# Optimization experiments

Hardware: AMD Instinct MI355X
Metric: run time of the kernel (lower is better)

Reference implementation:

```python
import jax, jax.numpy as jnp
import numpy as np

VOCAB_SIZE = 50000

def setup_inputs() -> dict:
    key = jax.random.key(0)
    # token index sequences: [batch, seq_len], values in [0, vocab)
    x = jax.random.randint(key, (2048, 200), 0, VOCAB_SIZE, dtype=jnp.int64)
    return {"x": x}

def reference(x) -> jnp.ndarray:
    # Faithful to: sum_{l} one_hot(x[b, l], V)  ->  [batch, vocab] count histogram.
    # Implemented as a scatter-add instead of materializing the
    # [batch, seq_len, vocab] one-hot tensor (same math, O(B*L) traffic on the
    # index side plus the [B, V] output).
    B, L = x.shape
    rows = jnp.broadcast_to(jnp.arange(B)[:, None], (B, L))  # [B, L]
    out = jnp.zeros((B, VOCAB_SIZE), dtype=jnp.float32)
    out = out.at[rows, x].add(jnp.float32(1.0))
    return out
```

## Files before the change

kernel.cpp:

```cpp
#include <hip/hip_runtime.h>
#include <hip/hip_bf16.h>

#define VOCAB   50000
#define SEQ     200
#define NCHUNK  4
#define CHUNK   (VOCAB / NCHUNK)
#define CDW     (CHUNK / 4)
#define CDW_PAD 3136

typedef float v4f __attribute__((ext_vector_type(4)));
typedef unsigned v4u __attribute__((ext_vector_type(4)));

__global__ __launch_bounds__(256) void MultihotEmbedding_16458314678493_kernel(
    const int* __restrict__ x, float* __restrict__ out) {
  __shared__ unsigned cnt[CDW_PAD];

  v4u* __restrict__ c4 = (v4u*)cnt;
  const v4u z = {0u, 0u, 0u, 0u};
  for (int i = threadIdx.x; i < CDW_PAD / 4; i += 256) c4[i] = z;
  __syncthreads();

  const int row = blockIdx.x >> 2;
  const int lo  = (blockIdx.x & 3) * CHUNK;
  const int* __restrict__ xr = x + row * SEQ;

  for (int t = threadIdx.x; t < SEQ; t += 256) {
    const int idx = xr[t] - lo;
    if ((unsigned)idx < (unsigned)CHUNK)
      atomicAdd(&cnt[idx >> 2], 1u << ((idx & 3) * 8));
  }
  __syncthreads();

  v4f* __restrict__ o4 = (v4f*)(out + (size_t)row * VOCAB + lo);
  for (int i = threadIdx.x; i < CDW; i += 256) {
    const unsigned u = cnt[i];
    v4f v;
    v.x = (float)(u & 0xffu);
    v.y = (float)((u >> 8) & 0xffu);
    v.z = (float)((u >> 16) & 0xffu);
    v.w = (float)(u >> 24);
    __builtin_nontemporal_store(v, &o4[i]);
  }
}

extern "C" void kernel_launch(void* const* d_in, const int* in_sizes, int n_in,
                              void* d_out, int out_size, void* d_ws, size_t ws_size,
                              hipStream_t stream) {
  const int* x = (const int*)d_in[0];
  float* out = (float*)d_out;
  const int batch = in_sizes[0] / SEQ;
  MultihotEmbedding_16458314678493_kernel<<<batch * NCHUNK, 256, 0, stream>>>(x, out);
}
```

Baseline: 415.7 us.

## Zero-fill output directly and scatter sparse counts instead of dense LDS conversion

Each thread now loads its token index at the start, so the global read overlaps with clearing the shared-memory counters. The dense output pass no longer reads and unpacks the packed byte counters from shared memory. Instead it stores constant zero vectors to the output slice, and after a barrier each thread writes the count for its own index as a scattered store. This takes shared-memory reads and unpacking off the bulk-store path. In exchange, the stores become regular rather than nontemporal, a second pass of scattered writes is added, and correctness relies on the barrier ordering the zero stores before the scattered writes within the block.

```diff
diff --git a/kernel.cpp b/kernel.cpp
--- a/kernel.cpp
+++ b/kernel.cpp
@@ -15,31 +15,30 @@
     const int* __restrict__ x, float* __restrict__ out) {
   __shared__ unsigned cnt[CDW_PAD];
 
+  const int row = blockIdx.x >> 2;
+  const int lo  = (blockIdx.x & 3) * CHUNK;
+
+  int myidx = CHUNK;
+  if (threadIdx.x < SEQ) myidx = x[row * SEQ + threadIdx.x] - lo;
+
   v4u* __restrict__ c4 = (v4u*)cnt;
-  const v4u z = {0u, 0u, 0u, 0u};
-  for (int i = threadIdx.x; i < CDW_PAD / 4; i += 256) c4[i] = z;
+  const v4u z4 = {0u, 0u, 0u, 0u};
+  for (int i = threadIdx.x; i < CDW_PAD / 4; i += 256) c4[i] = z4;
   __syncthreads();
 
-  const int row = blockIdx.x >> 2;
-  const int lo  = (blockIdx.x & 3) * CHUNK;
-  const int* __restrict__ xr = x + row * SEQ;
+  if ((unsigned)myidx < (unsigned)CHUNK)
+    atomicAdd(&cnt[myidx >> 2], 1u << ((myidx & 3) * 8));
 
-  for (int t = threadIdx.x; t < SEQ; t += 256) {
-    const int idx = xr[t] - lo;
-    if ((unsigned)idx < (unsigned)CHUNK)
-      atomicAdd(&cnt[idx >> 2], 1u << ((idx & 3) * 8));
-  }
+  float* __restrict__ orow = out + (size_t)row * VOCAB + lo;
+  v4f* __restrict__ o4 = (v4f*)orow;
+  const v4f zf = {0.f, 0.f, 0.f, 0.f};
+  #pragma unroll 4
+  for (int i = threadIdx.x; i < CDW; i += 256) o4[i] = zf;
   __syncthreads();
 
-  v4f* __restrict__ o4 = (v4f*)(out + (size_t)row * VOCAB + lo);
-  for (int i = threadIdx.x; i < CDW; i += 256) {
-    const unsigned u = cnt[i];
-    v4f v;
-    v.x = (float)(u & 0xffu);
-    v.y = (float)((u >> 8) & 0xffu);
-    v.z = (float)((u >> 16) & 0xffu);
-    v.w = (float)(u >> 24);
-    __builtin_nontemporal_store(v, &o4[i]);
+  if ((unsigned)myidx < (unsigned)CHUNK) {
+    const unsigned c = (cnt[myidx >> 2] >> ((myidx & 3) * 8)) & 0xffu;
+    orow[myidx] = (float)c;
   }
 }
 
```

Measured after the change: 410.8 us. Within noise of the previous version (-1.2%).
